# Kernel optimization log

Measured on AMD Instinct MI355X. Metric: run time of the kernel, lower is better.

The kernel has to match this reference:

```python
import jax, jax.numpy as jnp
import numpy as np

N_NODES = 100000
N_EDGES = 3200000
F_IN = 256
CUTOFF_DIST = 4.0
CUTOFF_ONSET = 3.8
D = 0.5 * (CUTOFF_DIST - CUTOFF_ONSET)  # 0.1
R = CUTOFF_DIST - D                      # 3.9


def setup_inputs() -> dict:
    key = jax.random.key(0)
    ks = jax.random.split(key, 8)
    node_features = jax.random.normal(ks[0], (N_NODES, F_IN), dtype=jnp.float32)
    bond_order = jax.random.uniform(ks[1], (N_EDGES,), dtype=jnp.float32)
    # scale to [0, 5) so the cutoff window [3.7, 4.1] is exercised
    bondlength = jax.random.uniform(ks[2], (N_EDGES,), dtype=jnp.float32) * 5.0
    src = jax.random.randint(ks[3], (N_EDGES,), 0, N_NODES, dtype=jnp.int64)
    dst = jax.random.randint(ks[4], (N_EDGES,), 0, N_NODES, dtype=jnp.int64)
    W_src = jax.random.normal(ks[5], (F_IN, 4), dtype=jnp.float32) * 0.05
    # bias init from the module: log([3264, 3.2394, 95.373, 1.3258])
    b_src = jnp.log(jnp.array([3264.0, 3.2394, 95.373, 1.3258], dtype=jnp.float32))
    W_dst = jax.random.normal(ks[6], (F_IN, 4), dtype=jnp.float32) * 0.05
    return {
        "node_features": node_features,
        "bond_order": bond_order,
        "bondlength": bondlength,
        "src": src,
        "dst": dst,
        "W_src": W_src,
        "b_src": b_src,
        "W_dst": W_dst,
    }


def _cutoff(r):
    c = jnp.where(r < R - D, 1.0, 0.5 - 0.5 * jnp.sin(jnp.pi * (r - R) / (2.0 * D)))
    return jnp.where(r > R + D, 0.0, c)


def reference(node_features, bond_order, bondlength, src, dst, W_src, b_src, W_dst):
    # per-node 4-vector projections
    e_src = node_features @ W_src + b_src          # [N, 4]
    e_dst = node_features @ W_dst                  # [N, 4]
    # gather to edges and combine (u_add_v), then exp
    params = jnp.exp(e_src[src] + e_dst[dst])      # [E, 4]
    f_repulse = params[:, 0] * jnp.exp(-params[:, 1] * bondlength)
    f_attract = params[:, 2] * jnp.exp(-params[:, 3] * bondlength)
    V_pair = _cutoff(bondlength) * (f_repulse - bond_order * f_attract)  # [E]
    # scatter-sum messages to destination nodes
    return jax.ops.segment_sum(V_pair, dst, num_segments=node_features.shape[0])
```

## Files before the change

### kernel.cpp

```cpp
#include <hip/hip_runtime.h>
#include <math.h>


#define F_IN 256
#define NB 49
#define BSH 11
#define BNODES 2048
#define SLOTS 16
#define NXCD 8
#define SC_T 512
#define SC_E 8
#define PBCAP 128

typedef float fx4 __attribute__((ext_vector_type(4)));
typedef int ix4 __attribute__((ext_vector_type(4)));
typedef unsigned ux2 __attribute__((ext_vector_type(2)));
typedef unsigned ux4 __attribute__((ext_vector_type(4)));

__device__ __forceinline__ unsigned xcc_id() {
  unsigned x;
  asm("s_getreg_b32 %0, hwreg(HW_REG_XCC_ID)" : "=s"(x));
  return x & (NXCD - 1);
}

__global__ __launch_bounds__(SC_T) void fused_kernel(
    const float* __restrict__ nf,
    const float* __restrict__ Wsrc,
    const float* __restrict__ bsrc,
    const float* __restrict__ Wdst,
    float* __restrict__ Psrc,
    float* __restrict__ Pdst,
    const float* __restrict__ bond_order,
    const float* __restrict__ bondlength,
    const int* __restrict__ src,
    const int* __restrict__ dst,
    ux2* __restrict__ region,
    unsigned* __restrict__ cntT,
    int n_nodes, int n_edges, int nsb, int npb) {
  __shared__ unsigned cnt[NB];
  __shared__ unsigned lofs[NB + 1];
  __shared__ ux2 stage[SC_T * SC_E];
  __shared__ unsigned char bkt8[SC_T * SC_E];

  const int bid = blockIdx.x;
  const int tid = threadIdx.x;
  const bool is_scatter = (nsb > 0) && (bid % 3 == 2);

  if (!is_scatter) {
    const int pidx = (nsb > 0) ? ((bid / 3) * 2 + (bid % 3)) : bid;
    if (pidx >= npb) return;
    const int gw = pidx * 8 + (tid >> 6);
    const int lane = tid & 63;
    const int node0 = gw * 8;
    if (node0 >= n_nodes) return;
    const int nm = min(8, n_nodes - node0);

    fx4 ws[4], wd[4];
#pragma unroll
    for (int t = 0; t < 4; ++t) {
      ws[t] = *reinterpret_cast<const fx4*>(Wsrc + (lane * 4 + t) * 4);
      wd[t] = *reinterpret_cast<const fx4*>(Wdst + (lane * 4 + t) * 4);
    }
    fx4 f[8];
#pragma unroll
    for (int m = 0; m < 8; ++m) {
      const int node = node0 + (m < nm ? m : 0);
      f[m] = __builtin_nontemporal_load(
          reinterpret_cast<const fx4*>(nf + (size_t)node * F_IN + lane * 4));
    }
    const int o = (lane & 1) * 4 + ((lane >> 1) & 1) * 2 + ((lane >> 2) & 1);
    const bool b1 = lane & 1, b2 = lane & 2, b4 = lane & 4;

#pragma unroll
    for (int m = 0; m < 8; ++m) {
      float a[8] = {0.f, 0.f, 0.f, 0.f, 0.f, 0.f, 0.f, 0.f};
#pragma unroll
      for (int t = 0; t < 4; ++t) {
        const float fv = f[m][t];
        a[0] += fv * ws[t].x; a[1] += fv * ws[t].y;
        a[2] += fv * ws[t].z; a[3] += fv * ws[t].w;
        a[4] += fv * wd[t].x; a[5] += fv * wd[t].y;
        a[6] += fv * wd[t].z; a[7] += fv * wd[t].w;
      }
      float s0 = b1 ? a[0] : a[4], s1 = b1 ? a[1] : a[5];
      float s2 = b1 ? a[2] : a[6], s3 = b1 ? a[3] : a[7];
      float r0 = __shfl_xor(s0, 1, 64), r1 = __shfl_xor(s1, 1, 64);
      float r2 = __shfl_xor(s2, 1, 64), r3 = __shfl_xor(s3, 1, 64);
      a[0] = (b1 ? a[4] : a[0]) + r0;
      a[1] = (b1 ? a[5] : a[1]) + r1;
      a[2] = (b1 ? a[6] : a[2]) + r2;
      a[3] = (b1 ? a[7] : a[3]) + r3;
      s0 = b2 ? a[0] : a[2]; s1 = b2 ? a[1] : a[3];
      r0 = __shfl_xor(s0, 2, 64); r1 = __shfl_xor(s1, 2, 64);
      a[0] = (b2 ? a[2] : a[0]) + r0;
      a[1] = (b2 ? a[3] : a[1]) + r1;
      s0 = b4 ? a[0] : a[1];
      r0 = __shfl_xor(s0, 4, 64);
      float v = (b4 ? a[1] : a[0]) + r0;
      v += __shfl_xor(v, 8, 64);
      v += __shfl_xor(v, 16, 64);
      v += __shfl_xor(v, 32, 64);

      if (m < nm && lane < 8) {
        const int node = node0 + m;
        if (o < 4) Psrc[(size_t)node * 4 + o] = __expf(v + bsrc[o]);
        else       Pdst[(size_t)node * 4 + (o - 4)] = __expf(v);
      }
    }
    return;
  }

  const int sblk = bid / 3;
  if (tid < NB) cnt[tid] = 0;
  __syncthreads();

  const long long e0 = (long long)sblk * (SC_T * SC_E) + (long long)tid * SC_E;
  float rr[SC_E], bb[SC_E];
  int sc[SC_E], dl[SC_E], bk[SC_E];
  unsigned rk[SC_E];
  bool act[SC_E];

  if (e0 + SC_E <= n_edges) {
    const fx4 r0 = __builtin_nontemporal_load(
        reinterpret_cast<const fx4*>(bondlength + e0));
    const fx4 r1 = __builtin_nontemporal_load(
        reinterpret_cast<const fx4*>(bondlength + e0 + 4));
    const fx4 b0 = __builtin_nontemporal_load(
        reinterpret_cast<const fx4*>(bond_order + e0));
    const fx4 b1 = __builtin_nontemporal_load(
        reinterpret_cast<const fx4*>(bond_order + e0 + 4));
    const ix4 s0 = __builtin_nontemporal_load(
        reinterpret_cast<const ix4*>(src + e0));
    const ix4 s1 = __builtin_nontemporal_load(
        reinterpret_cast<const ix4*>(src + e0 + 4));
    const ix4 d0 = __builtin_nontemporal_load(
        reinterpret_cast<const ix4*>(dst + e0));
    const ix4 d1 = __builtin_nontemporal_load(
        reinterpret_cast<const ix4*>(dst + e0 + 4));
#pragma unroll
    for (int j = 0; j < 4; ++j) {
      rr[j] = r0[j]; rr[j + 4] = r1[j];
      bb[j] = b0[j]; bb[j + 4] = b1[j];
      sc[j] = s0[j]; sc[j + 4] = s1[j];
      const int d = d0[j], dh = d1[j];
      bk[j] = d >> BSH; dl[j] = d & (BNODES - 1);
      bk[j + 4] = dh >> BSH; dl[j + 4] = dh & (BNODES - 1);
    }
  } else {
#pragma unroll
    for (int j = 0; j < SC_E; ++j) {
      rr[j] = 1.0e9f; bb[j] = 0.f; sc[j] = 0; bk[j] = 0; dl[j] = 0;
    }
    for (int j = 0; j < SC_E; ++j) {
      const long long e = e0 + j;
      if (e < n_edges) {
        rr[j] = bondlength[e];
        bb[j] = bond_order[e];
        sc[j] = src[e];
        const int d = dst[e];
        bk[j] = d >> BSH; dl[j] = d & (BNODES - 1);
      }
    }
  }

#pragma unroll
  for (int j = 0; j < SC_E; ++j) {
    act[j] = rr[j] < 4.0f;
    if (act[j]) rk[j] = atomicAdd(&cnt[bk[j]], 1u);
  }
  __syncthreads();

  if (tid == 0) {
    unsigned run = 0;
#pragma unroll
    for (int b = 0; b < NB; ++b) { lofs[b] = run; run += cnt[b]; }
    lofs[NB] = run;
  }
  __syncthreads();

#pragma unroll
  for (int j = 0; j < SC_E; ++j) {
    if (!act[j]) continue;
    unsigned ru = (unsigned)(rr[j] * 16384.0f + 0.5f);
    ru = ru > 65535u ? 65535u : ru;
    unsigned bu = (unsigned)(bb[j] * 65535.0f + 0.5f);
    bu = bu > 65535u ? 65535u : bu;
    ux2 rec;
    rec.x = ((unsigned)sc[j] << BSH) | (unsigned)dl[j];
    rec.y = (ru << 16) | bu;
    const unsigned sidx = lofs[bk[j]] + rk[j];
    stage[sidx] = rec;
    bkt8[sidx] = (unsigned char)bk[j];
  }
  __syncthreads();

  const unsigned total = lofs[NB];
  for (unsigned i = tid; i < total; i += SC_T) {
    const int b = bkt8[i];
    const unsigned pos = i - lofs[b];
    if (pos < PBCAP)
      region[((size_t)b * nsb + sblk) * PBCAP + pos] = stage[i];
  }
  if (tid < NB) cntT[(size_t)tid * nsb + sblk] = cnt[tid];
}

__global__ __launch_bounds__(256) void accum_kernel(
    const ux2* __restrict__ region,
    const unsigned* __restrict__ cntT,
    const fx4* __restrict__ Psrc,
    const fx4* __restrict__ Pdst,
    float* __restrict__ partial,
    int n_nodes, int nsb) {
  const int b = blockIdx.x / SLOTS;
  const int slot = blockIdx.x % SLOTS;
  __shared__ fx4 pdw[BNODES];
  __shared__ float acc[BNODES];
  const int tid = threadIdx.x;
  const int wv = tid >> 6, lane = tid & 63;
  const int nbase = b << BSH;

  for (int j = tid; j < BNODES; j += 256) {
    const int n = nbase + j;
    pdw[j] = (n < n_nodes) ? Pdst[n] : fx4{0.f, 0.f, 0.f, 0.f};
    acc[j] = 0.f;
  }
  __syncthreads();

  const unsigned* cb = cntT + (size_t)b * nsb;
  const ux2* rb = region + (size_t)b * nsb * PBCAP;

  for (int blk = slot * 4 + wv; blk < nsb; blk += SLOTS * 4) {
    const unsigned c = min(cb[blk], (unsigned)PBCAP);
    const unsigned i0 = 2u * (unsigned)lane;
    if (i0 >= c) continue;
    const ux4 rp = *reinterpret_cast<const ux4*>(rb + (size_t)blk * PBCAP + i0);
    const fx4 ps0 = Psrc[rp.x >> BSH];
    const bool h1 = (i0 + 1) < c;
    fx4 ps1;
    if (h1) ps1 = Psrc[rp.z >> BSH];

    {
      const int dl = rp.x & (BNODES - 1);
      const float r = (float)(rp.y >> 16) * (1.0f / 16384.0f);
      const float bo = (float)(rp.y & 0xffffu) * (1.0f / 65535.0f);
      const fx4 pd = pdw[dl];
      const float f_rep = (ps0.x * pd.x) * __expf(-(ps0.y * pd.y) * r);
      const float f_att = (ps0.z * pd.z) * __expf(-(ps0.w * pd.w) * r);
      float c1 = 1.0f;
      if (r > 3.8f) c1 = 0.5f - 0.5f * __sinf((float)M_PI * (r - 3.9f) * 5.0f);
      atomicAdd(&acc[dl], c1 * (f_rep - bo * f_att));
    }
    if (h1) {
      const int dl = rp.z & (BNODES - 1);
      const float r = (float)(rp.w >> 16) * (1.0f / 16384.0f);
      const float bo = (float)(rp.w & 0xffffu) * (1.0f / 65535.0f);
      const fx4 pd = pdw[dl];
      const float f_rep = (ps1.x * pd.x) * __expf(-(ps1.y * pd.y) * r);
      const float f_att = (ps1.z * pd.z) * __expf(-(ps1.w * pd.w) * r);
      float c1 = 1.0f;
      if (r > 3.8f) c1 = 0.5f - 0.5f * __sinf((float)M_PI * (r - 3.9f) * 5.0f);
      atomicAdd(&acc[dl], c1 * (f_rep - bo * f_att));
    }
  }
  __syncthreads();

  float* pout = partial + ((size_t)b * SLOTS + slot) * BNODES;
  for (int j = tid; j < BNODES; j += 256)
    __builtin_nontemporal_store(acc[j], pout + j);
}

__global__ __launch_bounds__(256) void reduce2_kernel(
    const float* __restrict__ partial, float* __restrict__ out, int n_nodes) {
  const int n = blockIdx.x * 256 + threadIdx.x;
  if (n >= n_nodes) return;
  const int b = n >> BSH;
  const int j = n & (BNODES - 1);
  const float* p = partial + (size_t)b * SLOTS * BNODES + j;
  float s = 0.f;
#pragma unroll
  for (int k = 0; k < SLOTS; ++k) s += p[(size_t)k * BNODES];
  out[n] = s;
}

__global__ __launch_bounds__(256) void edge_kernel_fb(
    const float* __restrict__ bond_order,
    const float* __restrict__ bondlength,
    const int* __restrict__ src,
    const int* __restrict__ dst,
    const fx4* __restrict__ Psrc,
    const fx4* __restrict__ Pdst,
    float* __restrict__ partial,
    int n_edges, int n_nodes) {
  float* myout = partial + (size_t)xcc_id() * n_nodes;
  const long long base = (long long)(blockIdx.x * blockDim.x + threadIdx.x) * 4;
  if (base >= n_edges) return;
  float rr[4], bb[4];
  int ss[4], dd[4];
  const int rem = (int)(((long long)n_edges - base) < 4 ? (n_edges - base) : 4);
  if (rem == 4) {
    const fx4 r4 = __builtin_nontemporal_load(
        reinterpret_cast<const fx4*>(bondlength + base));
    const fx4 b4 = __builtin_nontemporal_load(
        reinterpret_cast<const fx4*>(bond_order + base));
    const ix4 s4 = __builtin_nontemporal_load(
        reinterpret_cast<const ix4*>(src + base));
    const ix4 d4 = __builtin_nontemporal_load(
        reinterpret_cast<const ix4*>(dst + base));
#pragma unroll
    for (int j = 0; j < 4; ++j) {
      rr[j] = r4[j]; bb[j] = b4[j]; ss[j] = s4[j]; dd[j] = d4[j];
    }
  } else {
#pragma unroll
    for (int j = 0; j < 4; ++j) { rr[j] = 1e9f; bb[j] = 0.f; ss[j] = 0; dd[j] = 0; }
    for (int j = 0; j < rem; ++j) {
      rr[j] = bondlength[base + j]; bb[j] = bond_order[base + j];
      ss[j] = src[base + j]; dd[j] = dst[base + j];
    }
  }
#pragma unroll
  for (int j = 0; j < 4; ++j) {
    if (rr[j] >= 4.0f) continue;
    const fx4 es = Psrc[ss[j]];
    const fx4 ed = Pdst[dd[j]];
    const float r = rr[j];
    const float f_rep = (es.x * ed.x) * __expf(-(es.y * ed.y) * r);
    const float f_att = (es.z * ed.z) * __expf(-(es.w * ed.w) * r);
    float c = 1.0f;
    if (r > 3.8f) c = 0.5f - 0.5f * __sinf((float)M_PI * (r - 3.9f) * 5.0f);
    atomicAdd(&myout[dd[j]], c * (f_rep - bb[j] * f_att));
  }
}

__global__ __launch_bounds__(256) void reduce_fb_kernel(
    const float* __restrict__ partial, float* __restrict__ out, int n_nodes) {
  const int i = (blockIdx.x * blockDim.x + threadIdx.x) * 4;
  if (i >= n_nodes) return;
  if (i + 4 <= n_nodes) {
    fx4 s = *reinterpret_cast<const fx4*>(partial + i);
#pragma unroll
    for (int x = 1; x < NXCD; ++x)
      s += *reinterpret_cast<const fx4*>(partial + (size_t)x * n_nodes + i);
    *reinterpret_cast<fx4*>(out + i) = s;
  } else {
    for (int k = i; k < n_nodes; ++k) {
      float s = 0.f;
      for (int x = 0; x < NXCD; ++x) s += partial[(size_t)x * n_nodes + k];
      out[k] = s;
    }
  }
}

extern "C" void kernel_launch(void* const* d_in, const int* in_sizes, int n_in,
                              void* d_out, int out_size, void* d_ws,
                              size_t ws_size, hipStream_t stream) {
  const float* nf   = (const float*)d_in[0];
  const float* bo   = (const float*)d_in[1];
  const float* bl   = (const float*)d_in[2];
  const int*   src  = (const int*)d_in[3];
  const int*   dst  = (const int*)d_in[4];
  const float* Wsrc = (const float*)d_in[5];
  const float* bsrc = (const float*)d_in[6];
  const float* Wdst = (const float*)d_in[7];
  float* out = (float*)d_out;

  const int n_nodes = out_size;
  const int n_edges = in_sizes[1];

  const int nsb = (int)(((long long)n_edges + SC_T * SC_E - 1) / (SC_T * SC_E));
  const int npb = (n_nodes + 63) / 64;

  uint8_t* w = (uint8_t*)d_ws;
  const size_t pbytes = (size_t)n_nodes * 16;
  fx4* Psrc = (fx4*)w; w += pbytes;
  fx4* Pdst = (fx4*)w; w += pbytes;

  const size_t region_b  = (size_t)NB * nsb * PBCAP * 8;
  const size_t cnt_b     = ((size_t)NB * nsb * 4 + 255) & ~(size_t)255;
  const size_t partial_b = (size_t)NB * SLOTS * BNODES * 4;
  const size_t need = 2 * pbytes + region_b + cnt_b + partial_b + 256;
  const bool binned = (ws_size >= need) && (n_nodes <= NB * BNODES) &&
                      (n_nodes < (1 << 17));

  if (binned) {
    ux2* region = (ux2*)w; w += region_b;
    unsigned* cntT = (unsigned*)w; w += cnt_b;
    float* partial = (float*)w;

    {
      const int half = (npb + 1) / 2;
      const int grid = 3 * (nsb > half ? nsb : half);
      fused_kernel<<<grid, SC_T, 0, stream>>>(
          nf, Wsrc, bsrc, Wdst, (float*)Psrc, (float*)Pdst,
          bo, bl, src, dst, region, cntT, n_nodes, n_edges, nsb, npb);
    }
    accum_kernel<<<NB * SLOTS, 256, 0, stream>>>(region, cntT, Psrc, Pdst,
                                                 partial, n_nodes, nsb);
    reduce2_kernel<<<(n_nodes + 255) / 256, 256, 0, stream>>>(partial, out,
                                                              n_nodes);
  } else {
    float* partial = (float*)w;
    {
      fused_kernel<<<npb, SC_T, 0, stream>>>(
          nf, Wsrc, bsrc, Wdst, (float*)Psrc, (float*)Pdst,
          bo, bl, src, dst, nullptr, nullptr, n_nodes, n_edges, 0, npb);
    }
    (void)hipMemsetAsync(partial, 0, (size_t)NXCD * n_nodes * sizeof(float),
                         stream);
    {
      const long long threads = ((long long)n_edges + 3) / 4;
      const int blocks = (int)((threads + 255) / 256);
      edge_kernel_fb<<<blocks, 256, 0, stream>>>(bo, bl, src, dst, Psrc, Pdst,
                                                 partial, n_edges, n_nodes);
    }
    reduce_fb_kernel<<<(n_nodes + 1023) / 1024, 256, 0, stream>>>(partial, out,
                                                                  n_nodes);
  }
}
```

Measured before the change: 78.55 us.

## Fuse partial reduction into accum kernel via last-block counter; widen accum loads

Removes the separate reduce2 kernel: each accum block writes its partial, bumps a per-bin atomic counter, and the last of the SLOTS blocks for a bin sums the partials into the output. The counters are zeroed in the fused kernel. The accum loop now has each wave process a pair of bucket blocks with up to four records per lane, using nontemporal loads, so more gathers are in flight. This saves one kernel launch and exposes more memory-level parallelism, at the cost of a threadfence and atomic per block and a serialized tail reduction in the last block per bin.

```diff
diff --git a/kernel.cpp b/kernel.cpp
--- a/kernel.cpp
+++ b/kernel.cpp
@@ -15,7 +15,6 @@
 typedef float fx4 __attribute__((ext_vector_type(4)));
 typedef int ix4 __attribute__((ext_vector_type(4)));
 typedef unsigned ux2 __attribute__((ext_vector_type(2)));
-typedef unsigned ux4 __attribute__((ext_vector_type(4)));
 
 __device__ __forceinline__ unsigned xcc_id() {
   unsigned x;
@@ -36,6 +35,7 @@
     const int* __restrict__ dst,
     ux2* __restrict__ region,
     unsigned* __restrict__ cntT,
+    unsigned* __restrict__ done,
     int n_nodes, int n_edges, int nsb, int npb) {
   __shared__ unsigned cnt[NB];
   __shared__ unsigned lofs[NB + 1];
@@ -45,6 +45,8 @@
   const int bid = blockIdx.x;
   const int tid = threadIdx.x;
   const bool is_scatter = (nsb > 0) && (bid % 3 == 2);
+
+  if (done && bid == 0 && tid < NB) done[tid] = 0;
 
   if (!is_scatter) {
     const int pidx = (nsb > 0) ? ((bid / 3) * 2 + (bid % 3)) : bid;
@@ -210,11 +212,14 @@
     const fx4* __restrict__ Psrc,
     const fx4* __restrict__ Pdst,
     float* __restrict__ partial,
+    unsigned* __restrict__ done,
+    float* __restrict__ out,
     int n_nodes, int nsb) {
   const int b = blockIdx.x / SLOTS;
   const int slot = blockIdx.x % SLOTS;
   __shared__ fx4 pdw[BNODES];
   __shared__ float acc[BNODES];
+  __shared__ unsigned lastflag;
   const int tid = threadIdx.x;
   const int wv = tid >> 6, lane = tid & 63;
   const int nbase = b << BSH;
@@ -228,58 +233,69 @@
 
   const unsigned* cb = cntT + (size_t)b * nsb;
   const ux2* rb = region + (size_t)b * nsb * PBCAP;
-
-  for (int blk = slot * 4 + wv; blk < nsb; blk += SLOTS * 4) {
-    const unsigned c = min(cb[blk], (unsigned)PBCAP);
-    const unsigned i0 = 2u * (unsigned)lane;
-    if (i0 >= c) continue;
-    const ux4 rp = *reinterpret_cast<const ux4*>(rb + (size_t)blk * PBCAP + i0);
-    const fx4 ps0 = Psrc[rp.x >> BSH];
-    const bool h1 = (i0 + 1) < c;
-    fx4 ps1;
-    if (h1) ps1 = Psrc[rp.z >> BSH];
-
-    {
-      const int dl = rp.x & (BNODES - 1);
-      const float r = (float)(rp.y >> 16) * (1.0f / 16384.0f);
-      const float bo = (float)(rp.y & 0xffffu) * (1.0f / 65535.0f);
+  const int npairs = (nsb + 1) >> 1;
+
+  for (int p = slot * 4 + wv; p < npairs; p += SLOTS * 4) {
+    const int blkA = 2 * p, blkB = blkA + 1;
+    const unsigned cA = min(cb[blkA], (unsigned)PBCAP);
+    const unsigned cB = (blkB < nsb) ? min(cb[blkB], (unsigned)PBCAP) : 0u;
+    const unsigned ctot = cA + cB;
+
+    ux2 rec[4];
+    fx4 ps[4];
+    bool a[4];
+#pragma unroll
+    for (int rd = 0; rd < 4; ++rd) {
+      const unsigned v = (unsigned)lane + 64u * rd;
+      a[rd] = v < ctot;
+      if (a[rd]) {
+        const size_t idx = (v < cA)
+            ? ((size_t)blkA * PBCAP + v)
+            : ((size_t)blkB * PBCAP + (v - cA));
+        rec[rd] = __builtin_nontemporal_load(rb + idx);
+      }
+    }
+#pragma unroll
+    for (int rd = 0; rd < 4; ++rd)
+      if (a[rd]) ps[rd] = Psrc[rec[rd].x >> BSH];
+#pragma unroll
+    for (int rd = 0; rd < 4; ++rd) {
+      if (!a[rd]) continue;
+      const int dl = rec[rd].x & (BNODES - 1);
+      const float r = (float)(rec[rd].y >> 16) * (1.0f / 16384.0f);
+      const float bo = (float)(rec[rd].y & 0xffffu) * (1.0f / 65535.0f);
       const fx4 pd = pdw[dl];
-      const float f_rep = (ps0.x * pd.x) * __expf(-(ps0.y * pd.y) * r);
-      const float f_att = (ps0.z * pd.z) * __expf(-(ps0.w * pd.w) * r);
+      const float f_rep = (ps[rd].x * pd.x) * __expf(-(ps[rd].y * pd.y) * r);
+      const float f_att = (ps[rd].z * pd.z) * __expf(-(ps[rd].w * pd.w) * r);
       float c1 = 1.0f;
       if (r > 3.8f) c1 = 0.5f - 0.5f * __sinf((float)M_PI * (r - 3.9f) * 5.0f);
       atomicAdd(&acc[dl], c1 * (f_rep - bo * f_att));
     }
-    if (h1) {
-      const int dl = rp.z & (BNODES - 1);
-      const float r = (float)(rp.w >> 16) * (1.0f / 16384.0f);
-      const float bo = (float)(rp.w & 0xffffu) * (1.0f / 65535.0f);
-      const fx4 pd = pdw[dl];
-      const float f_rep = (ps1.x * pd.x) * __expf(-(ps1.y * pd.y) * r);
-      const float f_att = (ps1.z * pd.z) * __expf(-(ps1.w * pd.w) * r);
-      float c1 = 1.0f;
-      if (r > 3.8f) c1 = 0.5f - 0.5f * __sinf((float)M_PI * (r - 3.9f) * 5.0f);
-      atomicAdd(&acc[dl], c1 * (f_rep - bo * f_att));
-    }
   }
   __syncthreads();
 
   float* pout = partial + ((size_t)b * SLOTS + slot) * BNODES;
   for (int j = tid; j < BNODES; j += 256)
     __builtin_nontemporal_store(acc[j], pout + j);
-}
-
-__global__ __launch_bounds__(256) void reduce2_kernel(
-    const float* __restrict__ partial, float* __restrict__ out, int n_nodes) {
-  const int n = blockIdx.x * 256 + threadIdx.x;
-  if (n >= n_nodes) return;
-  const int b = n >> BSH;
-  const int j = n & (BNODES - 1);
-  const float* p = partial + (size_t)b * SLOTS * BNODES + j;
-  float s = 0.f;
-#pragma unroll
-  for (int k = 0; k < SLOTS; ++k) s += p[(size_t)k * BNODES];
-  out[n] = s;
+
+  __threadfence();
+  if (tid == 0) {
+    const unsigned prev = __hip_atomic_fetch_add(
+        &done[b], 1u, __ATOMIC_ACQ_REL, __HIP_MEMORY_SCOPE_AGENT);
+    lastflag = (prev == SLOTS - 1) ? 1u : 0u;
+  }
+  __syncthreads();
+  if (!lastflag) return;
+
+  const float* pb = partial + (size_t)b * SLOTS * BNODES;
+  for (int j = tid; j < BNODES; j += 256) {
+    const int n = nbase + j;
+    if (n >= n_nodes) continue;
+    float s = 0.f;
+#pragma unroll
+    for (int k = 0; k < SLOTS; ++k) s += pb[(size_t)k * BNODES + j];
+    out[n] = s;
+  }
 }
 
 __global__ __launch_bounds__(256) void edge_kernel_fb(
@@ -378,32 +394,34 @@
   const size_t region_b  = (size_t)NB * nsb * PBCAP * 8;
   const size_t cnt_b     = ((size_t)NB * nsb * 4 + 255) & ~(size_t)255;
   const size_t partial_b = (size_t)NB * SLOTS * BNODES * 4;
-  const size_t need = 2 * pbytes + region_b + cnt_b + partial_b + 256;
+  const size_t done_b    = 256;
+  const size_t need = 2 * pbytes + region_b + cnt_b + partial_b + done_b + 256;
   const bool binned = (ws_size >= need) && (n_nodes <= NB * BNODES) &&
                       (n_nodes < (1 << 17));
 
   if (binned) {
     ux2* region = (ux2*)w; w += region_b;
     unsigned* cntT = (unsigned*)w; w += cnt_b;
-    float* partial = (float*)w;
+    float* partial = (float*)w; w += partial_b;
+    unsigned* done = (unsigned*)w;
 
     {
       const int half = (npb + 1) / 2;
       const int grid = 3 * (nsb > half ? nsb : half);
       fused_kernel<<<grid, SC_T, 0, stream>>>(
           nf, Wsrc, bsrc, Wdst, (float*)Psrc, (float*)Pdst,
-          bo, bl, src, dst, region, cntT, n_nodes, n_edges, nsb, npb);
+          bo, bl, src, dst, region, cntT, done, n_nodes, n_edges, nsb, npb);
     }
     accum_kernel<<<NB * SLOTS, 256, 0, stream>>>(region, cntT, Psrc, Pdst,
-                                                 partial, n_nodes, nsb);
-    reduce2_kernel<<<(n_nodes + 255) / 256, 256, 0, stream>>>(partial, out,
-                                                              n_nodes);
+                                                 partial, done, out,
+                                                 n_nodes, nsb);
   } else {
     float* partial = (float*)w;
     {
       fused_kernel<<<npb, SC_T, 0, stream>>>(
           nf, Wsrc, bsrc, Wdst, (float*)Psrc, (float*)Pdst,
-          bo, bl, src, dst, nullptr, nullptr, n_nodes, n_edges, 0, npb);
+          bo, bl, src, dst, nullptr, nullptr, nullptr,
+          n_nodes, n_edges, 0, npb);
     }
     (void)hipMemsetAsync(partial, 0, (size_t)NXCD * n_nodes * sizeof(float),
                          stream);
```

After: 180.5 us. 130% more time.
